# Optimization experiments

Measured on AMD Instinct MI355X. Metric: run time of the kernel, lower is better.

Reference implementation:

```python
import jax, jax.numpy as jnp
import numpy as np

N_HEADS = 16


def setup_inputs() -> dict:
    key = jax.random.key(0)
    k1, k2, k3, k4 = jax.random.split(key, 4)
    B, T, C = 2, 2048, 1024
    x = jax.random.normal(k1, (B, T, C), dtype=jnp.float32)
    scale = 1.0 / np.sqrt(C)
    Wq = jax.random.normal(k2, (C, C), dtype=jnp.float32) * scale
    Wk = jax.random.normal(k3, (C, C), dtype=jnp.float32) * scale
    Wv = jax.random.normal(k4, (C, C), dtype=jnp.float32) * scale
    return {"x": x, "Wq": Wq, "Wk": Wk, "Wv": Wv}


def reference(x, Wq, Wk, Wv):
    B, T, C = x.shape
    H = N_HEADS
    Dh = C // H
    # Faithful to original: direct view of (B,T,C) -> (B,H,T,Dh) (no transpose)
    q = (x @ Wq.T).reshape(B, H, T, Dh)
    k = (x @ Wk.T).reshape(B, H, T, Dh)
    v = (x @ Wv.T).reshape(B, H, T, Dh)
    scores = jnp.einsum('bhqd,bhkd->bhqk', q, k) * (1.0 / (Dh ** 0.5))
    mask = jnp.tril(jnp.ones((T, T), dtype=bool))  # causal mask
    scores = jnp.where(mask, scores, -jnp.inf)
    att = jax.nn.softmax(scores, axis=-1)
    out = jnp.einsum('bhqk,bhkd->bhqd', att, v)
    return out.reshape(B, T, C)
```

## Files before the change

### kernel.cpp

```cpp
#include <hip/hip_runtime.h>
#include <hip/hip_bf16.h>
#include <stdint.h>

#define AS1 __attribute__((address_space(1)))
#define AS3 __attribute__((address_space(3)))

typedef __bf16 bf16x8 __attribute__((ext_vector_type(8)));
typedef float  f32x4  __attribute__((ext_vector_type(4)));
typedef unsigned short ushort8v __attribute__((ext_vector_type(8)));
typedef unsigned short ushort4v __attribute__((ext_vector_type(4)));
typedef short short8v __attribute__((ext_vector_type(8)));
typedef short short4v __attribute__((ext_vector_type(4)));

__device__ __forceinline__ unsigned short f2bf(float f) {
    unsigned int u = __float_as_uint(f);
    u += 0x7fffu + ((u >> 16) & 1u);
    return (unsigned short)(u >> 16);
}
__device__ __forceinline__ unsigned int pk2bf(float a, float b) {
    __hip_bfloat162 h = __float22bfloat162_rn(make_float2(a, b));
    unsigned int u;
    __builtin_memcpy(&u, &h, 4);
    return u;
}
__device__ __forceinline__ void g2lds16(const void* gp, void* lp) {
    __builtin_amdgcn_global_load_lds((AS1 void*)gp, (AS3 void*)lp, 16, 0, 0);
}
#define E2(x) __builtin_amdgcn_exp2f(x)

__global__ __launch_bounds__(256) void cast_all(const float* __restrict__ x,
                                                const float* __restrict__ w0,
                                                const float* __restrict__ w1,
                                                const float* __restrict__ w2,
                                                unsigned short* __restrict__ xb,
                                                unsigned short* __restrict__ wc) {
    int id = blockIdx.x;
    const float* s;
    unsigned short* d;
    int base;
    if (id < 4096) { s = x; d = xb; base = id; }
    else {
        int z = (id - 4096) >> 10;
        s = (z == 0) ? w0 : (z == 1) ? w1 : w2;
        d = wc + (size_t)z * 1048576;
        base = (id - 4096) & 1023;
    }
    int i = (base * 256 + threadIdx.x) * 4;
    float4 v = *(const float4*)(s + i);
    ushort4v o = { f2bf(v.x), f2bf(v.y), f2bf(v.z), f2bf(v.w) };
    *(ushort4v*)(d + i) = o;
}

#define VMW(n) asm volatile("s_waitcnt vmcnt(" #n ")" ::: "memory")
#define NOW
#define PHCORE(STG, MFMAS, ENDW) do {                                          \
    STG;                                                                       \
    __builtin_amdgcn_s_barrier();                                              \
    asm volatile("s_waitcnt lgkmcnt(0)" ::: "memory");                         \
    __builtin_amdgcn_sched_barrier(0);                                         \
    __builtin_amdgcn_s_setprio(1);                                             \
    MFMAS;                                                                     \
    __builtin_amdgcn_s_setprio(0);                                             \
    __builtin_amdgcn_sched_barrier(0);                                         \
    ENDW;                                                                      \
    __builtin_amdgcn_s_barrier();                                              \
} while (0)

#define PHA(S, CUR, STG, ENDW) do {                                            \
    const int kx_ = ((S) * 32 + quad * 8) ^ ((cl & 7) * 8);                    \
    bf16x8 af_[4];                                                             \
    _Pragma("unroll")                                                          \
    for (int m_ = 0; m_ < 4; ++m_)                                             \
        af_[m_] = *(const bf16x8*)&SA[CUR][(rowA0 + m_ * 16) * 64 + kx_];      \
    _Pragma("unroll")                                                          \
    for (int n_ = 0; n_ < 3; ++n_)                                             \
        bqr[n_] = *(const bf16x8*)&SB[CUR][(rowB0 + n_ * 16) * 64 + kx_];      \
    PHCORE(STG,                                                                \
        _Pragma("unroll")                                                      \
        for (int m_ = 0; m_ < 4; ++m_)                                         \
            _Pragma("unroll")                                                  \
            for (int n_ = 0; n_ < 3; ++n_)                                     \
                acc[m_][n_] = __builtin_amdgcn_mfma_f32_16x16x32_bf16(         \
                    af_[m_], bqr[n_], acc[m_][n_], 0, 0, 0);                   \
        , ENDW);                                                               \
} while (0)

#define PHB(S, CUR, STG, ENDW) do {                                            \
    const int kx_ = ((S) * 32 + quad * 8) ^ ((cl & 7) * 8);                    \
    bf16x8 af_[4];                                                             \
    _Pragma("unroll")                                                          \
    for (int m_ = 0; m_ < 4; ++m_)                                             \
        af_[m_] = *(const bf16x8*)&SA[CUR][(rowA0 + 64 + m_ * 16) * 64 + kx_]; \
    PHCORE(STG,                                                                \
        _Pragma("unroll")                                                      \
        for (int m_ = 0; m_ < 4; ++m_)                                         \
            _Pragma("unroll")                                                  \
            for (int n_ = 0; n_ < 3; ++n_)                                     \
                acc[4 + m_][n_] = __builtin_amdgcn_mfma_f32_16x16x32_bf16(     \
                    af_[m_], bqr[n_], acc[4 + m_][n_], 0, 0, 0);               \
        , ENDW);                                                               \
} while (0)

__global__ __launch_bounds__(512, 2) void gemm_qkv(const unsigned short* __restrict__ X,
                                                   const unsigned short* __restrict__ W,
                                                   unsigned short* __restrict__ QKV) {
    const int K = 1024;
    const int b = blockIdx.x;
    const int xcd = b & 7;
    const int j = b >> 3;
    const int m0 = (xcd * 2 + (j >> 4)) * 256;
    const int n0 = (j & 15) * 192;

    const float qs0 = 0.18033688011112042f;

    __shared__ unsigned short SA[2][16384];
    __shared__ unsigned short SB[2][12288];

    const int t = threadIdx.x;
    const int w = t >> 6;
    const int l = t & 63;
    const int cl = l & 15;
    const int quad = l >> 4;
    const int rowA0 = (w >> 2) * 128 + cl;
    const int rowB0 = (w & 3) * 48 + cl;

    const int srow8 = t >> 3;
    const int klog = (((t & 7) ^ ((t >> 3) & 7)) * 8);
    const unsigned short* Abase = X + (size_t)(m0 + srow8) * K + klog;
    const unsigned short* Bbase = W + (size_t)(n0 + srow8) * K + klog;
    unsigned short* const sa0 = &SA[0][w * 512];
    unsigned short* const sa1 = &SA[1][w * 512];
    unsigned short* const sb0 = &SB[0][w * 512];
    unsigned short* const sb1 = &SB[1][w * 512];

    f32x4 acc[8][3] = {};
    bf16x8 bqr[3];

#define STGA(nb, q, k0) g2lds16(Abase + (size_t)(q) * 65536 + (k0), ((nb) ? sa1 : sa0) + (q) * 4096)
#define STGB(nb, q, k0) g2lds16(Bbase + (size_t)(q) * 65536 + (k0), ((nb) ? sb1 : sb0) + (q) * 4096)

    STGB(0, 0, 0); STGB(0, 1, 0); STGB(0, 2, 0);
    STGA(0, 0, 0); STGA(0, 2, 0); STGA(0, 1, 0); STGA(0, 3, 0);
    VMW(2);
    __builtin_amdgcn_s_barrier();

    for (int tt = 0; tt < 15; ++tt) {
        const int cur = tt & 1, nxt = cur ^ 1;
        const int k1 = (tt + 1) * 64;
        PHA(0, cur, { STGB(nxt, 0, k1); STGB(nxt, 1, k1); STGB(nxt, 2, k1); STGA(nxt, 0, k1); }, VMW(4));
        PHB(0, cur, { STGA(nxt, 2, k1); STGA(nxt, 1, k1); STGA(nxt, 3, k1); }, NOW);
        PHA(1, cur, {}, NOW);
        PHB(1, cur, {}, VMW(2));
    }
    PHA(0, 1, {}, VMW(0));
    PHB(0, 1, {}, NOW);
    PHA(1, 1, {}, NOW);
    PHB(1, 1, {}, NOW);

#undef STGA
#undef STGB

    #pragma unroll
    for (int mf = 0; mf < 8; ++mf) {
        #pragma unroll
        for (int rr = 0; rr < 4; ++rr) {
            size_t row = (size_t)(m0 + (w >> 2) * 128 + mf * 16 + quad * 4 + rr);
            #pragma unroll
            for (int nf = 0; nf < 3; ++nf) {
                const int nbase = n0 + (w & 3) * 48 + nf * 16;
                const int z = nbase >> 10;
                const float qs = (z == 0) ? qs0 : 1.0f;
                unsigned short* Cz = QKV + (size_t)z * 4194304;
                Cz[row * 1024 + ((nbase & 1023) + cl)] = f2bf(acc[mf][nf][rr] * qs);
            }
        }
    }
}

__global__ __launch_bounds__(256) void vtrans(const unsigned short* __restrict__ Vn,
                                              unsigned short* __restrict__ V3) {
    const int bh = blockIdx.y;
    const int T0 = blockIdx.x * 128;
    __shared__ unsigned short L[128 * 72];
    const int t = threadIdx.x;

    const unsigned short* src = Vn + (size_t)bh * 131072 + (size_t)T0 * 64;
    #pragma unroll
    for (int p = 0; p < 4; ++p) {
        int r = p * 32 + (t >> 3), c = (t & 7) * 8;
        *(ushort8v*)(L + r * 72 + c) = *(const ushort8v*)(src + (size_t)r * 64 + c);
    }
    __syncthreads();
    unsigned short* dst = V3 + (size_t)bh * 131072 + (size_t)(T0 >> 4) * 1024;
    #pragma unroll
    for (int p = 0; p < 2; ++p) {
        int item = p * 256 + t;
        int kb = item >> 6, cl = (item >> 2) & 15, qk = item & 3;
        ushort8v a, b;
        #pragma unroll
        for (int u = 0; u < 8; ++u) {
            int dt = u >> 2, j = u & 3;
            a[u] = L[(kb * 16 + qk * 4 + j) * 72 + dt * 16 + cl];
            b[u] = L[(kb * 16 + qk * 4 + j) * 72 + (dt + 2) * 16 + cl];
        }
        unsigned short* dp = dst + kb * 1024 + cl * 64 + qk * 16;
        *(ushort8v*)(dp) = a;
        *(ushort8v*)(dp + 8) = b;
    }
}

__global__ __launch_bounds__(256, 4) void attn(const unsigned short* __restrict__ QK,
                                               const unsigned short* __restrict__ V3,
                                               float* __restrict__ Out) {
    const int id = blockIdx.x;
    const int g = id & 255;
    const int s4 = id >> 8;
    const int bh = g & 31;
    const int pp = g >> 5;
    const int bb = (s4 == 0) ? (31 - pp)
                 : (s4 == 1) ? pp
                 : (s4 == 2) ? (23 - pp)
                             : (8 + pp);
    const int t = threadIdx.x;
    const int w = t >> 6;
    const int l = t & 63;
    const int cl = l & 15;
    const int quad = l >> 4;
    const int c7 = cl & 7;

    const size_t bhoff = (size_t)bh * 131072;
    const unsigned short* Qb = QK + bhoff;
    const unsigned short* Kb = QK + (size_t)4194304 + bhoff;
    const unsigned short* Vb = V3 + bhoff;
    float* Ob = Out + bhoff;

    __shared__ unsigned short KVs[2][8192];

    const int g2 = t + 256;
    const int kO1 = (t >> 3) * 64 + (((t & 7) ^ ((t >> 3) & 7)) * 8);
    const int kO2 = (g2 >> 3) * 64 + (((g2 & 7) ^ ((g2 >> 3) & 7)) * 8);
    const int wg1 = t & 63;
    const int wg2 = g2 & 63;
    const int vO1 = (t >> 6) * 512 + ((wg1 ^ ((wg1 >> 3) & 7)) * 8);
    const int vO2 = (g2 >> 6) * 512 + ((wg2 ^ ((wg2 >> 3) & 7)) * 8);
    const int lB1 = w * 512;
    const int lB2 = 2048 + w * 512;

    const int oK0 = cl * 64 + (((quad)     ^ c7) * 8);
    const int oK1 = cl * 64 + (((quad + 4) ^ c7) * 8);
    const int oV0 = cl * 64 + (((quad * 2)     ^ c7) * 8);
    const int oV1 = cl * 64 + (((quad * 2 + 1) ^ c7) * 8);

    const int mrel = w * 16 + cl;
    const int nch = bb + 1;
    const int m0w = bb * 64 + w * 16;

    bf16x8 qf0, qf1;
    {
        const unsigned short* qa = Qb + (size_t)(m0w + cl) * 64 + quad * 8;
        qf0 = *(const bf16x8*)(qa);
        qf1 = *(const bf16x8*)(qa + 32);
    }

    f32x4 o[4] = {};
    float lps = 0.f;

    {
        unsigned short* s = &KVs[0][0];
        g2lds16(Kb + kO1, s + lB1);
        g2lds16(Kb + kO2, s + lB2);
        g2lds16(Vb + vO1, s + 4096 + lB1);
        g2lds16(Vb + vO2, s + 4096 + lB2);
    }

    for (int c = 0; c < nch; ++c) {
        __syncthreads();
        if (c + 1 < nch) {
            unsigned short* s = &KVs[(c + 1) & 1][0];
            const size_t off = (size_t)(c + 1) * 4096;
            g2lds16(Kb + off + kO1, s + lB1);
            g2lds16(Kb + off + kO2, s + lB2);
            g2lds16(Vb + off + vO1, s + 4096 + lB1);
            g2lds16(Vb + off + vO2, s + 4096 + lB2);
        }
        const unsigned short* Kl = &KVs[c & 1][0];
        const unsigned short* Vl = Kl + 4096;
        const bool masked = (c == bb);

        bf16x8 kf0[4], kf1[4];
        #pragma unroll
        for (int kt = 0; kt < 4; ++kt) {
            kf0[kt] = *(const bf16x8*)(Kl + kt * 1024 + oK0);
            kf1[kt] = *(const bf16x8*)(Kl + kt * 1024 + oK1);
        }
        f32x4 st[4] = {};
        __builtin_amdgcn_s_setprio(1);
        #pragma unroll
        for (int kt = 0; kt < 4; ++kt) {
            st[kt] = __builtin_amdgcn_mfma_f32_16x16x32_bf16(kf0[kt], qf0, st[kt], 0, 0, 0);
            st[kt] = __builtin_amdgcn_mfma_f32_16x16x32_bf16(kf1[kt], qf1, st[kt], 0, 0, 0);
        }
        __builtin_amdgcn_s_setprio(0);

        short4v pb[4];
        #pragma unroll
        for (int kt = 0; kt < 4; ++kt) {
            float p0, p1, p2, p3;
            if (masked) {
                const int lk = kt * 16 + quad * 4;
                p0 = (lk     <= mrel) ? E2(st[kt][0]) : 0.f;
                p1 = (lk + 1 <= mrel) ? E2(st[kt][1]) : 0.f;
                p2 = (lk + 2 <= mrel) ? E2(st[kt][2]) : 0.f;
                p3 = (lk + 3 <= mrel) ? E2(st[kt][3]) : 0.f;
            } else {
                p0 = E2(st[kt][0]);
                p1 = E2(st[kt][1]);
                p2 = E2(st[kt][2]);
                p3 = E2(st[kt][3]);
            }
            lps += (p0 + p1) + (p2 + p3);
            uint2 u = { pk2bf(p0, p1), pk2bf(p2, p3) };
            short4v pv;
            __builtin_memcpy(&pv, &u, 8);
            pb[kt] = pv;
        }

        __builtin_amdgcn_s_setprio(1);
        #pragma unroll
        for (int kt = 0; kt < 4; ++kt) {
            short8v v0 = *(const short8v*)(Vl + kt * 1024 + oV0);
            short8v v1 = *(const short8v*)(Vl + kt * 1024 + oV1);
            short4v a0 = __builtin_shufflevector(v0, v0, 0, 1, 2, 3);
            short4v a1 = __builtin_shufflevector(v0, v0, 4, 5, 6, 7);
            short4v a2 = __builtin_shufflevector(v1, v1, 0, 1, 2, 3);
            short4v a3 = __builtin_shufflevector(v1, v1, 4, 5, 6, 7);
            o[0] = __builtin_amdgcn_mfma_f32_16x16x16bf16_1k(a0, pb[kt], o[0], 0, 0, 0);
            o[1] = __builtin_amdgcn_mfma_f32_16x16x16bf16_1k(a1, pb[kt], o[1], 0, 0, 0);
            o[2] = __builtin_amdgcn_mfma_f32_16x16x16bf16_1k(a2, pb[kt], o[2], 0, 0, 0);
            o[3] = __builtin_amdgcn_mfma_f32_16x16x16bf16_1k(a3, pb[kt], o[3], 0, 0, 0);
        }
        __builtin_amdgcn_s_setprio(0);
    }

    lps += __shfl_xor(lps, 16);
    lps += __shfl_xor(lps, 32);
    const float inv = 1.0f / lps;
    #pragma unroll
    for (int dt = 0; dt < 4; ++dt) {
        f32x4 r = o[dt];
        r[0] *= inv; r[1] *= inv; r[2] *= inv; r[3] *= inv;
        *(f32x4*)(Ob + (size_t)(m0w + cl) * 64 + dt * 16 + quad * 4) = r;
    }
}

extern "C" void kernel_launch(void* const* d_in, const int* in_sizes, int n_in,
                              void* d_out, int out_size, void* d_ws, size_t ws_size,
                              hipStream_t stream) {
    const float* x  = (const float*)d_in[0];
    const float* Wq = (const float*)d_in[1];
    const float* Wk = (const float*)d_in[2];
    const float* Wv = (const float*)d_in[3];
    float* out = (float*)d_out;

    unsigned short* xb  = (unsigned short*)d_ws;
    unsigned short* wc  = xb + (size_t)4096 * 1024;
    unsigned short* qkv = wc + (size_t)3 * 1024 * 1024;
    unsigned short* vt  = qkv + (size_t)3 * 4096 * 1024;

    hipLaunchKernelGGL(cast_all, dim3(7168), dim3(256), 0, stream, x, Wq, Wk, Wv, xb, wc);
    hipLaunchKernelGGL(gemm_qkv, dim3(256), dim3(512), 0, stream, xb, wc, qkv);
    hipLaunchKernelGGL(vtrans, dim3(16, 32), dim3(256), 0, stream, qkv + (size_t)2 * 4096 * 1024, vt);
    hipLaunchKernelGGL(attn, dim3(1024), dim3(256), 0, stream, qkv, vt, out);
}
```

Before: 139.1 us.

## Switch attention to 32x32x16 MFMA with two-wave blocks and new V layout

Rewrites the attention kernel to use 32x32x16 bf16 MFMAs, with each wave covering 32 query rows instead of 16 and blocks of 128 threads instead of 256. vtrans now writes V in a layout matched to the 32x32 B-operand, and the P fragments are rearranged between half-waves with cross-lane shuffles. The aim is fewer MFMA issues and LDS reads per FLOP. In exchange each block carries more registers per thread (two 16-float accumulators for S and two for O), and each thread now issues twice as many global-to-LDS loads.

```diff
diff --git a/kernel.cpp b/kernel.cpp
--- a/kernel.cpp
+++ b/kernel.cpp
@@ -7,6 +7,7 @@
 
 typedef __bf16 bf16x8 __attribute__((ext_vector_type(8)));
 typedef float  f32x4  __attribute__((ext_vector_type(4)));
+typedef float  f32x16 __attribute__((ext_vector_type(16)));
 typedef unsigned short ushort8v __attribute__((ext_vector_type(8)));
 typedef unsigned short ushort4v __attribute__((ext_vector_type(4)));
 typedef short short8v __attribute__((ext_vector_type(8)));
@@ -178,7 +179,7 @@
 }
 
 __global__ __launch_bounds__(256) void vtrans(const unsigned short* __restrict__ Vn,
-                                              unsigned short* __restrict__ V3) {
+                                              unsigned short* __restrict__ V32) {
     const int bh = blockIdx.y;
     const int T0 = blockIdx.x * 128;
     __shared__ unsigned short L[128 * 72];
@@ -191,26 +192,24 @@
         *(ushort8v*)(L + r * 72 + c) = *(const ushort8v*)(src + (size_t)r * 64 + c);
     }
     __syncthreads();
-    unsigned short* dst = V3 + (size_t)bh * 131072 + (size_t)(T0 >> 4) * 1024;
-    #pragma unroll
-    for (int p = 0; p < 2; ++p) {
-        int item = p * 256 + t;
-        int kb = item >> 6, cl = (item >> 2) & 15, qk = item & 3;
-        ushort8v a, b;
-        #pragma unroll
-        for (int u = 0; u < 8; ++u) {
-            int dt = u >> 2, j = u & 3;
-            a[u] = L[(kb * 16 + qk * 4 + j) * 72 + dt * 16 + cl];
-            b[u] = L[(kb * 16 + qk * 4 + j) * 72 + (dt + 2) * 16 + cl];
-        }
-        unsigned short* dp = dst + kb * 1024 + cl * 64 + qk * 16;
-        *(ushort8v*)(dp) = a;
-        *(ushort8v*)(dp + 8) = b;
-    }
-}
-
-__global__ __launch_bounds__(256, 4) void attn(const unsigned short* __restrict__ QK,
-                                               const unsigned short* __restrict__ V3,
+    unsigned short* dst = V32 + (size_t)bh * 131072 + (size_t)(T0 >> 6) * 4096;
+    #pragma unroll
+    for (int cc = 0; cc < 2; ++cc) {
+        #pragma unroll
+        for (int p = 0; p < 2; ++p) {
+            int i = p * 256 + t;
+            int kvb = i >> 7, dblk = (i >> 6) & 1, h = (i >> 5) & 1, dl = i & 31;
+            ushort8v a;
+            #pragma unroll
+            for (int jj = 0; jj < 8; ++jj)
+                a[jj] = L[(cc * 64 + kvb * 16 + h * 8 + jj) * 72 + dblk * 32 + dl];
+            *(ushort8v*)(dst + cc * 4096 + i * 8) = a;
+        }
+    }
+}
+
+__global__ __launch_bounds__(128, 2) void attn(const unsigned short* __restrict__ QK,
+                                               const unsigned short* __restrict__ V32,
                                                float* __restrict__ Out) {
     const int id = blockIdx.x;
     const int g = id & 255;
@@ -224,132 +223,139 @@
     const int t = threadIdx.x;
     const int w = t >> 6;
     const int l = t & 63;
-    const int cl = l & 15;
-    const int quad = l >> 4;
-    const int c7 = cl & 7;
+    const int q32 = l & 31;
+    const int h = l >> 5;
 
     const size_t bhoff = (size_t)bh * 131072;
     const unsigned short* Qb = QK + bhoff;
     const unsigned short* Kb = QK + (size_t)4194304 + bhoff;
-    const unsigned short* Vb = V3 + bhoff;
+    const unsigned short* Vb = V32 + bhoff;
     float* Ob = Out + bhoff;
 
     __shared__ unsigned short KVs[2][8192];
 
-    const int g2 = t + 256;
-    const int kO1 = (t >> 3) * 64 + (((t & 7) ^ ((t >> 3) & 7)) * 8);
-    const int kO2 = (g2 >> 3) * 64 + (((g2 & 7) ^ ((g2 >> 3) & 7)) * 8);
-    const int wg1 = t & 63;
-    const int wg2 = g2 & 63;
-    const int vO1 = (t >> 6) * 512 + ((wg1 ^ ((wg1 >> 3) & 7)) * 8);
-    const int vO2 = (g2 >> 6) * 512 + ((wg2 ^ ((wg2 >> 3) & 7)) * 8);
-    const int lB1 = w * 512;
-    const int lB2 = 2048 + w * 512;
-
-    const int oK0 = cl * 64 + (((quad)     ^ c7) * 8);
-    const int oK1 = cl * 64 + (((quad + 4) ^ c7) * 8);
-    const int oV0 = cl * 64 + (((quad * 2)     ^ c7) * 8);
-    const int oV1 = cl * 64 + (((quad * 2 + 1) ^ c7) * 8);
-
-    const int mrel = w * 16 + cl;
+    int kOi[4];
+    #pragma unroll
+    for (int i = 0; i < 4; ++i) {
+        int gi = i * 128 + t;
+        kOi[i] = (gi >> 3) * 64 + (((gi & 7) ^ ((gi >> 3) & 7)) * 8);
+    }
+    const int vsrc0 = t * 8;
+    const int lB = w * 512;
+
     const int nch = bb + 1;
-    const int m0w = bb * 64 + w * 16;
-
-    bf16x8 qf0, qf1;
+    const int qbase = bb * 64 + w * 32;
+    const int mrel = w * 32 + q32;
+
+    bf16x8 qf[4];
     {
-        const unsigned short* qa = Qb + (size_t)(m0w + cl) * 64 + quad * 8;
-        qf0 = *(const bf16x8*)(qa);
-        qf1 = *(const bf16x8*)(qa + 32);
-    }
-
-    f32x4 o[4] = {};
+        const unsigned short* qa = Qb + (size_t)(qbase + q32) * 64 + h * 8;
+        #pragma unroll
+        for (int db = 0; db < 4; ++db)
+            qf[db] = *(const bf16x8*)(qa + db * 16);
+    }
+
+    f32x16 o0 = {}, o1 = {};
     float lps = 0.f;
 
-    {
-        unsigned short* s = &KVs[0][0];
-        g2lds16(Kb + kO1, s + lB1);
-        g2lds16(Kb + kO2, s + lB2);
-        g2lds16(Vb + vO1, s + 4096 + lB1);
-        g2lds16(Vb + vO2, s + 4096 + lB2);
-    }
+#define STGC(cc, buf) do {                                                     \
+    unsigned short* s_ = &KVs[buf][0];                                         \
+    const size_t off_ = (size_t)(cc) * 4096;                                   \
+    _Pragma("unroll")                                                          \
+    for (int i_ = 0; i_ < 4; ++i_) {                                           \
+        g2lds16(Kb + off_ + kOi[i_], s_ + i_ * 1024 + lB);                     \
+        g2lds16(Vb + off_ + i_ * 1024 + vsrc0, s_ + 4096 + i_ * 1024 + lB);    \
+    }                                                                          \
+} while (0)
+
+    STGC(0, 0);
 
     for (int c = 0; c < nch; ++c) {
         __syncthreads();
-        if (c + 1 < nch) {
-            unsigned short* s = &KVs[(c + 1) & 1][0];
-            const size_t off = (size_t)(c + 1) * 4096;
-            g2lds16(Kb + off + kO1, s + lB1);
-            g2lds16(Kb + off + kO2, s + lB2);
-            g2lds16(Vb + off + vO1, s + 4096 + lB1);
-            g2lds16(Vb + off + vO2, s + 4096 + lB2);
-        }
+        if (c + 1 < nch) STGC(c + 1, (c + 1) & 1);
         const unsigned short* Kl = &KVs[c & 1][0];
         const unsigned short* Vl = Kl + 4096;
         const bool masked = (c == bb);
 
         bf16x8 kf0[4], kf1[4];
         #pragma unroll
-        for (int kt = 0; kt < 4; ++kt) {
-            kf0[kt] = *(const bf16x8*)(Kl + kt * 1024 + oK0);
-            kf1[kt] = *(const bf16x8*)(Kl + kt * 1024 + oK1);
-        }
-        f32x4 st[4] = {};
+        for (int db = 0; db < 4; ++db) {
+            const int kx = (db * 16 + h * 8) ^ ((l & 7) * 8);
+            kf0[db] = *(const bf16x8*)(Kl + (q32) * 64 + kx);
+            kf1[db] = *(const bf16x8*)(Kl + (32 + q32) * 64 + kx);
+        }
+        f32x16 st0 = {}, st1 = {};
         __builtin_amdgcn_s_setprio(1);
         #pragma unroll
-        for (int kt = 0; kt < 4; ++kt) {
-            st[kt] = __builtin_amdgcn_mfma_f32_16x16x32_bf16(kf0[kt], qf0, st[kt], 0, 0, 0);
-            st[kt] = __builtin_amdgcn_mfma_f32_16x16x32_bf16(kf1[kt], qf1, st[kt], 0, 0, 0);
+        for (int db = 0; db < 4; ++db) {
+            st0 = __builtin_amdgcn_mfma_f32_32x32x16_bf16(kf0[db], qf[db], st0, 0, 0, 0);
+            st1 = __builtin_amdgcn_mfma_f32_32x32x16_bf16(kf1[db], qf[db], st1, 0, 0, 0);
         }
         __builtin_amdgcn_s_setprio(0);
 
-        short4v pb[4];
-        #pragma unroll
-        for (int kt = 0; kt < 4; ++kt) {
-            float p0, p1, p2, p3;
-            if (masked) {
-                const int lk = kt * 16 + quad * 4;
-                p0 = (lk     <= mrel) ? E2(st[kt][0]) : 0.f;
-                p1 = (lk + 1 <= mrel) ? E2(st[kt][1]) : 0.f;
-                p2 = (lk + 2 <= mrel) ? E2(st[kt][2]) : 0.f;
-                p3 = (lk + 3 <= mrel) ? E2(st[kt][3]) : 0.f;
-            } else {
-                p0 = E2(st[kt][0]);
-                p1 = E2(st[kt][1]);
-                p2 = E2(st[kt][2]);
-                p3 = E2(st[kt][3]);
+        unsigned int u[2][8];
+        #pragma unroll
+        for (int kvblk = 0; kvblk < 2; ++kvblk) {
+            const f32x16 stx = kvblk ? st1 : st0;
+            #pragma unroll
+            for (int s = 0; s < 8; ++s) {
+                float pa, pbv;
+                {
+                    const int r = 2 * s;
+                    const int kvloc = kvblk * 32 + 4 * h + (r & 3) + 8 * (r >> 2);
+                    pa = (!masked || kvloc <= mrel) ? E2(stx[r]) : 0.f;
+                }
+                {
+                    const int r = 2 * s + 1;
+                    const int kvloc = kvblk * 32 + 4 * h + (r & 3) + 8 * (r >> 2);
+                    pbv = (!masked || kvloc <= mrel) ? E2(stx[r]) : 0.f;
+                }
+                lps += pa + pbv;
+                u[kvblk][s] = pk2bf(pa, pbv);
             }
-            lps += (p0 + p1) + (p2 + p3);
-            uint2 u = { pk2bf(p0, p1), pk2bf(p2, p3) };
-            short4v pv;
-            __builtin_memcpy(&pv, &u, 8);
-            pb[kt] = pv;
+        }
+
+        bf16x8 pb[4];
+        #pragma unroll
+        for (int kvb = 0; kvb < 4; ++kvb) {
+            const int kb = kvb >> 1, b1 = kvb & 1;
+            const unsigned int A0 = u[kb][4 * b1 + 0], A1 = u[kb][4 * b1 + 1];
+            const unsigned int B0 = u[kb][4 * b1 + 2], B1 = u[kb][4 * b1 + 3];
+            const unsigned int s0 = h ? A0 : B0;
+            const unsigned int s1 = h ? A1 : B1;
+            const unsigned int r0 = (unsigned int)__shfl_xor((int)s0, 32);
+            const unsigned int r1 = (unsigned int)__shfl_xor((int)s1, 32);
+            unsigned int vals[4];
+            vals[0] = h ? r0 : A0;
+            vals[1] = h ? r1 : A1;
+            vals[2] = h ? B0 : r0;
+            vals[3] = h ? B1 : r1;
+            __builtin_memcpy(&pb[kvb], vals, 16);
         }
 
         __builtin_amdgcn_s_setprio(1);
         #pragma unroll
-        for (int kt = 0; kt < 4; ++kt) {
-            short8v v0 = *(const short8v*)(Vl + kt * 1024 + oV0);
-            short8v v1 = *(const short8v*)(Vl + kt * 1024 + oV1);
-            short4v a0 = __builtin_shufflevector(v0, v0, 0, 1, 2, 3);
-            short4v a1 = __builtin_shufflevector(v0, v0, 4, 5, 6, 7);
-            short4v a2 = __builtin_shufflevector(v1, v1, 0, 1, 2, 3);
-            short4v a3 = __builtin_shufflevector(v1, v1, 4, 5, 6, 7);
-            o[0] = __builtin_amdgcn_mfma_f32_16x16x16bf16_1k(a0, pb[kt], o[0], 0, 0, 0);
-            o[1] = __builtin_amdgcn_mfma_f32_16x16x16bf16_1k(a1, pb[kt], o[1], 0, 0, 0);
-            o[2] = __builtin_amdgcn_mfma_f32_16x16x16bf16_1k(a2, pb[kt], o[2], 0, 0, 0);
-            o[3] = __builtin_amdgcn_mfma_f32_16x16x16bf16_1k(a3, pb[kt], o[3], 0, 0, 0);
+        for (int kvb = 0; kvb < 4; ++kvb) {
+            const bf16x8 vfa = *(const bf16x8*)(Vl + kvb * 1024 + h * 256 + q32 * 8);
+            const bf16x8 vfb = *(const bf16x8*)(Vl + kvb * 1024 + 512 + h * 256 + q32 * 8);
+            o0 = __builtin_amdgcn_mfma_f32_32x32x16_bf16(vfa, pb[kvb], o0, 0, 0, 0);
+            o1 = __builtin_amdgcn_mfma_f32_32x32x16_bf16(vfb, pb[kvb], o1, 0, 0, 0);
         }
         __builtin_amdgcn_s_setprio(0);
     }
-
-    lps += __shfl_xor(lps, 16);
+#undef STGC
+
     lps += __shfl_xor(lps, 32);
     const float inv = 1.0f / lps;
-    #pragma unroll
-    for (int dt = 0; dt < 4; ++dt) {
-        f32x4 r = o[dt];
-        r[0] *= inv; r[1] *= inv; r[2] *= inv; r[3] *= inv;
-        *(f32x4*)(Ob + (size_t)(m0w + cl) * 64 + dt * 16 + quad * 4) = r;
+    float* const ob = Ob + (size_t)(qbase + q32) * 64 + 4 * h;
+    #pragma unroll
+    for (int rq = 0; rq < 4; ++rq) {
+        f32x4 ra = { o0[rq * 4 + 0] * inv, o0[rq * 4 + 1] * inv,
+                     o0[rq * 4 + 2] * inv, o0[rq * 4 + 3] * inv };
+        *(f32x4*)(ob + 8 * rq) = ra;
+        f32x4 rb = { o1[rq * 4 + 0] * inv, o1[rq * 4 + 1] * inv,
+                     o1[rq * 4 + 2] * inv, o1[rq * 4 + 3] * inv };
+        *(f32x4*)(ob + 32 + 8 * rq) = rb;
     }
 }
 
@@ -370,5 +376,5 @@
     hipLaunchKernelGGL(cast_all, dim3(7168), dim3(256), 0, stream, x, Wq, Wk, Wv, xb, wc);
     hipLaunchKernelGGL(gemm_qkv, dim3(256), dim3(512), 0, stream, xb, wc, qkv);
     hipLaunchKernelGGL(vtrans, dim3(16, 32), dim3(256), 0, stream, qkv + (size_t)2 * 4096 * 1024, vt);
-    hipLaunchKernelGGL(attn, dim3(1024), dim3(256), 0, stream, qkv, vt, out);
-}
+    hipLaunchKernelGGL(attn, dim3(1024), dim3(128), 0, stream, qkv, vt, out);
+}
```

Result: slower. 149.3 us (+7.4%).
